# Kernel tuning notes

Measured on AMD Instinct MI355X. Metric: run time of the kernel, lower is better.

The kernel has to match this reference:

```python
import jax, jax.numpy as jnp
import numpy as np

IN_C = 128
KEY_C = 128
VAL_C = 128
HEADS = 8
N_CLS = 4

def setup_inputs() -> dict:
    key = jax.random.key(0)
    ks = jax.random.split(key, 10)
    n, c, d, h, w = 2, IN_C, 16, 64, 64
    x = jax.random.normal(ks[0], (n, c, d, h, w), dtype=jnp.float32)
    CLS = jax.random.normal(ks[1], (n, KEY_C, N_CLS), dtype=jnp.float32)
    s = 0.02
    Wk = jax.random.normal(ks[2], (KEY_C, IN_C), dtype=jnp.float32) * s
    bk = jnp.zeros((KEY_C,), dtype=jnp.float32)
    Wq = jax.random.normal(ks[3], (KEY_C, IN_C), dtype=jnp.float32) * s
    bq = jnp.zeros((KEY_C,), dtype=jnp.float32)
    Wv = jax.random.normal(ks[4], (VAL_C, IN_C), dtype=jnp.float32) * s
    bv = jnp.zeros((VAL_C,), dtype=jnp.float32)
    Wr = jax.random.normal(ks[5], (IN_C, VAL_C), dtype=jnp.float32) * s
    br = jnp.zeros((IN_C,), dtype=jnp.float32)
    return {"x": x, "CLS": CLS, "Wk": Wk, "bk": bk, "Wq": Wq, "bq": bq,
            "Wv": Wv, "bv": bv, "Wr": Wr, "br": br}

def reference(x, CLS, Wk, bk, Wq, bq, Wv, bv, Wr, br):
    n, c, d, h, w = x.shape
    L = d * h * w
    xf = x.reshape(n, c, L)
    # 1x1 Conv3d == channel matmul
    keys = jnp.einsum('oc,ncl->nol', Wk, xf) + bk[None, :, None]
    queries = jnp.einsum('oc,ncl->nol', Wq, xf) + bq[None, :, None]
    values = jnp.einsum('oc,ncl->nol', Wv, xf) + bv[None, :, None]
    # prepend CLS tokens along the sequence axis
    keys = jnp.concatenate([CLS, keys], axis=-1)      # (n, kc, L+4)
    queries = jnp.concatenate([CLS, queries], axis=-1)
    values = jnp.concatenate([CLS, values], axis=-1)
    Lt = L + N_CLS
    hk = KEY_C // HEADS
    hv = VAL_C // HEADS
    # contiguous channel slices per head == reshape (n, HEADS, hk, Lt)
    k = jax.nn.softmax(keys.reshape(n, HEADS, hk, Lt), axis=3)    # softmax over sequence
    q = jax.nn.softmax(queries.reshape(n, HEADS, hk, Lt), axis=2) # softmax over head channels
    v = values.reshape(n, HEADS, hv, Lt)
    context = jnp.einsum('nhkl,nhvl->nhkv', k, v)                 # (n, H, hk, hv)
    att = jnp.einsum('nhkv,nhkl->nhvl', context, q)               # (n, H, hv, Lt)
    # original loop reassigns CLS each head; final value comes from last head
    CLS_out = att[:, -1, :, :N_CLS]                               # (n, hv, 4)
    agg = att[:, :, :, N_CLS:].reshape(n, HEADS * hv, L)          # concat over heads
    attention = (jnp.einsum('oc,ncl->nol', Wr, agg) + br[None, :, None]).reshape(n, c, d, h, w)
    context_last = context[:, -1]                                 # last head's context
    return (attention, context_last, CLS_out)
```

## Files before the change

kernel.cpp:

```cpp
#include <hip/hip_runtime.h>

typedef unsigned short u16;
typedef short bf16x8 __attribute__((ext_vector_type(8)));
typedef float floatx4 __attribute__((ext_vector_type(4)));

#define L_TOT 65536
#define OUT_CTX 16777216
#define OUT_CLS (OUT_CTX + 512)

__device__ __forceinline__ u16 f2b(float f) {
  unsigned int u = __float_as_uint(f);
  u += 0x7fffu + ((u >> 16) & 1u);
  return (u16)(u >> 16);
}
__device__ __forceinline__ float blo(unsigned int u) { return __uint_as_float(u << 16); }
__device__ __forceinline__ float bhi(unsigned int u) { return __uint_as_float(u & 0xffff0000u); }

__device__ __forceinline__ float pack_val(const float* W, int eo) {
  int mt = eo >> 11;
  int rem = eo & 2047;
  int ks = rem >> 9;
  int lane = (rem >> 3) & 63;
  int j = rem & 7;
  int row = mt * 16 + (lane & 15);
  int col = ks * 32 + (lane >> 4) * 8 + j;
  return W[row * 128 + col];
}

__global__ __launch_bounds__(256) void kP(
    const float* __restrict__ Wk, const float* __restrict__ Wq,
    const float* __restrict__ Wv, const float* __restrict__ Wr,
    const float* __restrict__ CLS,
    float* __restrict__ S2, float* __restrict__ Cnum2,
    u16* __restrict__ wkv, u16* __restrict__ wqf, u16* __restrict__ wrf) {
  const int t = threadIdx.x;
  if (blockIdx.x < 32) {
    #pragma unroll
    for (int i = 0; i < 8; ++i) {
      int e = blockIdx.x * 2048 + i * 256 + t;
      if (e < 32768) {
        wkv[e] = f2b(pack_val(e < 16384 ? Wk : Wv, e & 16383));
      } else if (e < 49152) {
        int eq = e - 32768;
        wqf[eq] = f2b(pack_val(Wq, eq));
      } else {
        int er = e - 49152;
        wrf[er] = f2b(pack_val(Wr, er));
      }
    }
  } else {
    int n = t >> 7, r = t & 127;
    float s = 0.f;
    #pragma unroll
    for (int j = 0; j < 4; ++j) s += __expf(CLS[(n * 128 + r) * 4 + j]);
    S2[n * 128 + r] = s;
    S2[256 + n * 128 + r] = 0.f;
    for (int i = 0; i < 16; ++i) {
      int o = t * 16 + i;
      int nn = o >> 11;
      int rem = o & 2047;
      int h = rem >> 8;
      int kc = (rem >> 4) & 15;
      int vc = rem & 15;
      float a = 0.f;
      #pragma unroll
      for (int j = 0; j < 4; ++j)
        a += __expf(CLS[(nn * 128 + h * 16 + kc) * 4 + j]) *
             CLS[(nn * 128 + h * 16 + vc) * 4 + j];
      Cnum2[o] = a;
      Cnum2[4096 + o] = 0.f;
    }
  }
}

__global__ __launch_bounds__(256) void kA(
    const float* __restrict__ x, const float* __restrict__ bk,
    const float* __restrict__ bv, float* __restrict__ S2,
    float* __restrict__ Cnum2, const u16* __restrict__ wkv) {
  __shared__ __align__(16) u16 xT[64][136];
  __shared__ __align__(16) u16 ev[256][72];
  const int t = threadIdx.x;
  const int w = t >> 6, lane = t & 63;
  const int quad = lane >> 4, lm = lane & 15;
  const int n = blockIdx.x >> 8;
  const int l0base = (blockIdx.x & 255) << 8;
  const int slot = blockIdx.x & 1;

  const int sc = t >> 4;
  const int sl4 = t & 15;

  float4 pf[8];
  #pragma unroll
  for (int i = 0; i < 8; ++i) {
    int c = i * 16 + sc;
    pf[i] = *(const float4*)(x + (((size_t)(n * 128 + c)) << 16) + l0base + sl4 * 4);
  }

  bf16x8 wf[4][4];
  #pragma unroll
  for (int mt = 0; mt < 4; ++mt) {
    int rb = (mt < 2) ? (2 * w + mt) : (8 + 2 * w + (mt - 2));
    #pragma unroll
    for (int ks = 0; ks < 4; ++ks)
      wf[mt][ks] = *(const bf16x8*)(wkv + (((rb * 4 + ks) * 64 + lane) * 8));
  }
  float bias_[4][4];
  #pragma unroll
  for (int mt = 0; mt < 4; ++mt)
    #pragma unroll
    for (int j = 0; j < 4; ++j) {
      int r = w * 32 + (mt & 1) * 16 + quad * 4 + j;
      bias_[mt][j] = (mt < 2) ? bk[r] : bv[r];
    }

  floatx4 z4 = {0.f, 0.f, 0.f, 0.f};
  floatx4 cacc[2] = {z4, z4};
  float sacc = 0.f;

  for (int tile = 0; tile < 4; ++tile) {
    #pragma unroll
    for (int i = 0; i < 8; ++i) {
      int cc = i * 16 + sc;
      int col = sl4 * 4;
      xT[col + 0][cc] = f2b(pf[i].x);
      xT[col + 1][cc] = f2b(pf[i].y);
      xT[col + 2][cc] = f2b(pf[i].z);
      xT[col + 3][cc] = f2b(pf[i].w);
    }
    __syncthreads();

    floatx4 acc[4][4];
    #pragma unroll
    for (int mt = 0; mt < 4; ++mt)
      #pragma unroll
      for (int nt = 0; nt < 4; ++nt) acc[mt][nt] = z4;

    #pragma unroll
    for (int nt = 0; nt < 4; ++nt)
      #pragma unroll
      for (int ks = 0; ks < 4; ++ks) {
        bf16x8 b = *(const bf16x8*)(&xT[nt * 16 + lm][ks * 32 + quad * 8]);
        #pragma unroll
        for (int mt = 0; mt < 4; ++mt)
          acc[mt][nt] = __builtin_amdgcn_mfma_f32_16x16x32_bf16(wf[mt][ks], b, acc[mt][nt], 0, 0, 0);
      }

    #pragma unroll
    for (int mt = 0; mt < 4; ++mt)
      #pragma unroll
      for (int j = 0; j < 4; ++j) {
        int R = ((mt < 2) ? 0 : 128) + w * 32 + (mt & 1) * 16 + quad * 4 + j;
        #pragma unroll
        for (int nt = 0; nt < 4; ++nt) {
          float v = acc[mt][nt][j] + bias_[mt][j];
          if (mt < 2) v = __expf(v);
          ev[R][nt * 16 + lm] = f2b(v);
        }
      }

    if (tile < 3) {
      int l0 = l0base + (tile + 1) * 64;
      #pragma unroll
      for (int i = 0; i < 8; ++i) {
        int c = i * 16 + sc;
        pf[i] = *(const float4*)(x + (((size_t)(n * 128 + c)) << 16) + l0 + sl4 * 4);
      }
    }
    __syncthreads();

    #pragma unroll
    for (int hh = 0; hh < 2; ++hh) {
      int h = w * 2 + hh;
      #pragma unroll
      for (int ks = 0; ks < 2; ++ks) {
        bf16x8 aE = *(const bf16x8*)(&ev[h * 16 + lm][ks * 32 + quad * 8]);
        bf16x8 bV = *(const bf16x8*)(&ev[128 + h * 16 + lm][ks * 32 + quad * 8]);
        cacc[hh] = __builtin_amdgcn_mfma_f32_16x16x32_bf16(aE, bV, cacc[hh], 0, 0, 0);
      }
    }
    if (t < 128) {
      #pragma unroll
      for (int i = 0; i < 8; ++i) {
        uint4 u = *(const uint4*)(&ev[t][i * 8]);
        sacc += blo(u.x) + bhi(u.x) + blo(u.y) + bhi(u.y) +
                blo(u.z) + bhi(u.z) + blo(u.w) + bhi(u.w);
      }
    }
  }

  float* Cn = Cnum2 + slot * 4096;
  #pragma unroll
  for (int hh = 0; hh < 2; ++hh) {
    int h = w * 2 + hh;
    #pragma unroll
    for (int j = 0; j < 4; ++j)
      atomicAdd(&Cn[((n * 8 + h) * 16 + quad * 4 + j) * 16 + lm], cacc[hh][j]);
  }
  if (t < 128) atomicAdd(&S2[slot * 256 + n * 128 + t], sacc);
}

__global__ __launch_bounds__(256) void kB(
    const float* __restrict__ x, const float* __restrict__ bq,
    const float* __restrict__ br, const u16* __restrict__ wqf,
    const u16* __restrict__ wrf, const float* __restrict__ S2,
    const float* __restrict__ Cnum2, const float* __restrict__ CLS,
    float* __restrict__ out) {
  __shared__ __align__(16) u16 xT[64][136];
  __shared__ __align__(16) u16 qT[64][136];
  __shared__ __align__(16) u16 aT[64][136];
  const int t = threadIdx.x;
  const int w = t >> 6, lane = t & 63;
  const int quad = lane >> 4, lm = lane & 15;
  const int n = blockIdx.x >> 8;
  const int l0base = (blockIdx.x & 255) << 8;

  const int sc = t >> 4;
  const int sl4 = t & 15;

  float4 pf[8];
  #pragma unroll
  for (int i = 0; i < 8; ++i) {
    int c = i * 16 + sc;
    pf[i] = *(const float4*)(x + (((size_t)(n * 128 + c)) << 16) + l0base + sl4 * 4);
  }

  bf16x8 wq[2][4], wr[2][4];
  #pragma unroll
  for (int mt = 0; mt < 2; ++mt)
    #pragma unroll
    for (int ks = 0; ks < 4; ++ks) {
      wq[mt][ks] = *(const bf16x8*)(wqf + ((((w * 2 + mt) * 4 + ks) * 64 + lane) * 8));
      wr[mt][ks] = *(const bf16x8*)(wrf + ((((w * 2 + mt) * 4 + ks) * 64 + lane) * 8));
    }

  bf16x8 aC[2];
  #pragma unroll
  for (int mt = 0; mt < 2; ++mt) {
    int h = w * 2 + mt;
    short frag[8];
    #pragma unroll
    for (int j = 0; j < 8; ++j) {
      int k = quad * 8 + j;
      float v = 0.f;
      if (k < 16) {
        int ci = ((n * 8 + h) * 16 + k) * 16 + lm;
        float c = Cnum2[ci] + Cnum2[4096 + ci];
        float s = S2[n * 128 + h * 16 + k] + S2[256 + n * 128 + h * 16 + k];
        v = c / s;
      }
      frag[j] = (short)f2b(v);
    }
    aC[mt] = *(bf16x8*)frag;
  }

  if (blockIdx.x == 0) {
    for (int e = t; e < 512; e += 256) {
      int nn = e >> 8;
      int kc = (e >> 4) & 15;
      int vc = e & 15;
      int ci = ((nn * 8 + 7) * 16 + kc) * 16 + vc;
      float c = Cnum2[ci] + Cnum2[4096 + ci];
      float s = S2[nn * 128 + 112 + kc] + S2[256 + nn * 128 + 112 + kc];
      out[OUT_CTX + e] = c / s;
    }
    if (t < 128) {
      int nn = t >> 6;
      int vc = (t >> 2) & 15;
      int j = t & 3;
      float den = 0.f, num = 0.f;
      #pragma unroll
      for (int kc = 0; kc < 16; ++kc) {
        float e_ = __expf(CLS[(nn * 128 + 112 + kc) * 4 + j]);
        int ci = ((nn * 8 + 7) * 16 + kc) * 16 + vc;
        float c = Cnum2[ci] + Cnum2[4096 + ci];
        float s = S2[nn * 128 + 112 + kc] + S2[256 + nn * 128 + 112 + kc];
        den += e_;
        num += e_ * (c / s);
      }
      out[OUT_CLS + t] = num / den;
    }
  }

  float bqv_[2][4], brv[2][4];
  #pragma unroll
  for (int mt = 0; mt < 2; ++mt)
    #pragma unroll
    for (int j = 0; j < 4; ++j) {
      bqv_[mt][j] = bq[(w * 2 + mt) * 16 + quad * 4 + j];
      brv[mt][j] = br[(w * 2 + mt) * 16 + quad * 4 + j];
    }

  floatx4 z4 = {0.f, 0.f, 0.f, 0.f};

  for (int tile = 0; tile < 4; ++tile) {
    int l0 = l0base + tile * 64;
    #pragma unroll
    for (int i = 0; i < 8; ++i) {
      int cc = i * 16 + sc;
      int col = sl4 * 4;
      xT[col + 0][cc] = f2b(pf[i].x);
      xT[col + 1][cc] = f2b(pf[i].y);
      xT[col + 2][cc] = f2b(pf[i].z);
      xT[col + 3][cc] = f2b(pf[i].w);
    }
    __syncthreads();

    floatx4 acc[2][4];
    #pragma unroll
    for (int mt = 0; mt < 2; ++mt)
      #pragma unroll
      for (int nt = 0; nt < 4; ++nt) acc[mt][nt] = z4;

    #pragma unroll
    for (int nt = 0; nt < 4; ++nt)
      #pragma unroll
      for (int ks = 0; ks < 4; ++ks) {
        bf16x8 b = *(const bf16x8*)(&xT[nt * 16 + lm][ks * 32 + quad * 8]);
        #pragma unroll
        for (int mt = 0; mt < 2; ++mt)
          acc[mt][nt] = __builtin_amdgcn_mfma_f32_16x16x32_bf16(wq[mt][ks], b, acc[mt][nt], 0, 0, 0);
      }

    #pragma unroll
    for (int mt = 0; mt < 2; ++mt) {
      int h = w * 2 + mt;
      #pragma unroll
      for (int nt = 0; nt < 4; ++nt) {
        float e[4];
        float ssum = 0.f;
        #pragma unroll
        for (int j = 0; j < 4; ++j) {
          e[j] = __expf(acc[mt][nt][j] + bqv_[mt][j]);
          ssum += e[j];
        }
        ssum += __shfl_xor(ssum, 16);
        ssum += __shfl_xor(ssum, 32);
        float inv = 1.f / ssum;
        #pragma unroll
        for (int j = 0; j < 4; ++j)
          qT[nt * 16 + lm][h * 16 + quad * 4 + j] = f2b(e[j] * inv);
      }
    }

    #pragma unroll
    for (int mt = 0; mt < 2; ++mt) {
      int h = w * 2 + mt;
      #pragma unroll
      for (int nt = 0; nt < 4; ++nt) {
        bf16x8 bq_ = *(const bf16x8*)(&qT[nt * 16 + lm][h * 16 + (quad & 1) * 8]);
        floatx4 d = __builtin_amdgcn_mfma_f32_16x16x32_bf16(aC[mt], bq_, z4, 0, 0, 0);
        #pragma unroll
        for (int j = 0; j < 4; ++j)
          aT[nt * 16 + lm][h * 16 + quad * 4 + j] = f2b(d[j]);
      }
    }

    if (tile < 3) {
      int l0n = l0base + (tile + 1) * 64;
      #pragma unroll
      for (int i = 0; i < 8; ++i) {
        int c = i * 16 + sc;
        pf[i] = *(const float4*)(x + (((size_t)(n * 128 + c)) << 16) + l0n + sl4 * 4);
      }
    }
    __syncthreads();

    floatx4 acc2[2][4];
    #pragma unroll
    for (int mt = 0; mt < 2; ++mt)
      #pragma unroll
      for (int nt = 0; nt < 4; ++nt) acc2[mt][nt] = z4;

    #pragma unroll
    for (int nt = 0; nt < 4; ++nt)
      #pragma unroll
      for (int ks = 0; ks < 4; ++ks) {
        bf16x8 b = *(const bf16x8*)(&aT[nt * 16 + lm][ks * 32 + quad * 8]);
        #pragma unroll
        for (int mt = 0; mt < 2; ++mt)
          acc2[mt][nt] = __builtin_amdgcn_mfma_f32_16x16x32_bf16(wr[mt][ks], b, acc2[mt][nt], 0, 0, 0);
      }

    #pragma unroll
    for (int mt = 0; mt < 2; ++mt)
      #pragma unroll
      for (int j = 0; j < 4; ++j) {
        int R = (w * 2 + mt) * 16 + quad * 4 + j;
        #pragma unroll
        for (int nt = 0; nt < 4; ++nt)
          out[(((size_t)(n * 128 + R)) << 16) + l0 + nt * 16 + lm] = acc2[mt][nt][j] + brv[mt][j];
      }
  }
}

extern "C" void kernel_launch(void* const* d_in, const int* in_sizes, int n_in,
                              void* d_out, int out_size, void* d_ws, size_t ws_size,
                              hipStream_t stream) {
  const float* x   = (const float*)d_in[0];
  const float* CLS = (const float*)d_in[1];
  const float* Wk  = (const float*)d_in[2];
  const float* bk  = (const float*)d_in[3];
  const float* Wq  = (const float*)d_in[4];
  const float* bq  = (const float*)d_in[5];
  const float* Wv  = (const float*)d_in[6];
  const float* bv  = (const float*)d_in[7];
  const float* Wr  = (const float*)d_in[8];
  const float* br  = (const float*)d_in[9];
  float* out = (float*)d_out;
  char* ws = (char*)d_ws;
  float* S2    = (float*)(ws + 0);
  float* Cnum2 = (float*)(ws + 2048);
  u16* wkv     = (u16*)(ws + 34816);
  u16* wqf     = (u16*)(ws + 100352);
  u16* wrf     = (u16*)(ws + 133120);

  kP<<<33, 256, 0, stream>>>(Wk, Wq, Wv, Wr, CLS, S2, Cnum2, wkv, wqf, wrf);
  kA<<<512, 256, 0, stream>>>(x, bk, bv, S2, Cnum2, wkv);
  kB<<<512, 256, 0, stream>>>(x, bq, br, wqf, wrf, S2, Cnum2, CLS, out);
}
```

Before: 168.7 us.

## Fold context into output projection and double block count for attention kernels

Adds a small kernel kM that normalizes the accumulated context and folds it into the output projection weights (Wr·context per batch). This removes kB's per-tile context MFMA and the aT shared buffer, so the second GEMM consumes the softmaxed queries directly. Both main kernels now launch 1024 blocks of 128 positions each instead of 512 blocks of 256, with four atomic slots instead of two. kA computes the key-exp row sums from registers with shuffle reductions rather than rereading shared memory, and double-buffers xT so one barrier per tile can be dropped. The cost is an extra kernel launch and more atomics into four slots.

```diff
diff --git a/kernel.cpp b/kernel.cpp
--- a/kernel.cpp
+++ b/kernel.cpp
@@ -4,7 +4,6 @@
 typedef short bf16x8 __attribute__((ext_vector_type(8)));
 typedef float floatx4 __attribute__((ext_vector_type(4)));
 
-#define L_TOT 65536
 #define OUT_CTX 16777216
 #define OUT_CLS (OUT_CTX + 512)
 
@@ -13,8 +12,7 @@
   u += 0x7fffu + ((u >> 16) & 1u);
   return (u16)(u >> 16);
 }
-__device__ __forceinline__ float blo(unsigned int u) { return __uint_as_float(u << 16); }
-__device__ __forceinline__ float bhi(unsigned int u) { return __uint_as_float(u & 0xffff0000u); }
+__device__ __forceinline__ float b2f(u16 b) { return __uint_as_float(((unsigned int)b) << 16); }
 
 __device__ __forceinline__ float pack_val(const float* W, int eo) {
   int mt = eo >> 11;
@@ -29,35 +27,32 @@
 
 __global__ __launch_bounds__(256) void kP(
     const float* __restrict__ Wk, const float* __restrict__ Wq,
-    const float* __restrict__ Wv, const float* __restrict__ Wr,
-    const float* __restrict__ CLS,
+    const float* __restrict__ Wv, const float* __restrict__ CLS,
     float* __restrict__ S2, float* __restrict__ Cnum2,
-    u16* __restrict__ wkv, u16* __restrict__ wqf, u16* __restrict__ wrf) {
+    u16* __restrict__ wkv, u16* __restrict__ wqf) {
   const int t = threadIdx.x;
-  if (blockIdx.x < 32) {
+  if (blockIdx.x < 24) {
     #pragma unroll
     for (int i = 0; i < 8; ++i) {
       int e = blockIdx.x * 2048 + i * 256 + t;
       if (e < 32768) {
         wkv[e] = f2b(pack_val(e < 16384 ? Wk : Wv, e & 16383));
-      } else if (e < 49152) {
-        int eq = e - 32768;
-        wqf[eq] = f2b(pack_val(Wq, eq));
       } else {
-        int er = e - 49152;
-        wrf[er] = f2b(pack_val(Wr, er));
+        wqf[e - 32768] = f2b(pack_val(Wq, e - 32768));
       }
     }
   } else {
-    int n = t >> 7, r = t & 127;
+    int nn = t >> 7, r = t & 127;
     float s = 0.f;
     #pragma unroll
-    for (int j = 0; j < 4; ++j) s += __expf(CLS[(n * 128 + r) * 4 + j]);
-    S2[n * 128 + r] = s;
-    S2[256 + n * 128 + r] = 0.f;
+    for (int j = 0; j < 4; ++j) s += __expf(CLS[(nn * 128 + r) * 4 + j]);
+    S2[t] = s;
+    S2[256 + t] = 0.f;
+    S2[512 + t] = 0.f;
+    S2[768 + t] = 0.f;
     for (int i = 0; i < 16; ++i) {
       int o = t * 16 + i;
-      int nn = o >> 11;
+      int n2 = o >> 11;
       int rem = o & 2047;
       int h = rem >> 8;
       int kc = (rem >> 4) & 15;
@@ -65,10 +60,12 @@
       float a = 0.f;
       #pragma unroll
       for (int j = 0; j < 4; ++j)
-        a += __expf(CLS[(nn * 128 + h * 16 + kc) * 4 + j]) *
-             CLS[(nn * 128 + h * 16 + vc) * 4 + j];
+        a += __expf(CLS[(n2 * 128 + h * 16 + kc) * 4 + j]) *
+             CLS[(n2 * 128 + h * 16 + vc) * 4 + j];
       Cnum2[o] = a;
       Cnum2[4096 + o] = 0.f;
+      Cnum2[8192 + o] = 0.f;
+      Cnum2[12288 + o] = 0.f;
     }
   }
 }
@@ -77,15 +74,14 @@
     const float* __restrict__ x, const float* __restrict__ bk,
     const float* __restrict__ bv, float* __restrict__ S2,
     float* __restrict__ Cnum2, const u16* __restrict__ wkv) {
-  __shared__ __align__(16) u16 xT[64][136];
+  __shared__ __align__(16) u16 xT[2][64][136];
   __shared__ __align__(16) u16 ev[256][72];
   const int t = threadIdx.x;
   const int w = t >> 6, lane = t & 63;
   const int quad = lane >> 4, lm = lane & 15;
-  const int n = blockIdx.x >> 8;
-  const int l0base = (blockIdx.x & 255) << 8;
-  const int slot = blockIdx.x & 1;
-
+  const int n = blockIdx.x >> 9;
+  const int l0base = (blockIdx.x & 511) << 7;
+  const int slot = blockIdx.x & 3;
   const int sc = t >> 4;
   const int sl4 = t & 15;
 
@@ -115,9 +111,193 @@
 
   floatx4 z4 = {0.f, 0.f, 0.f, 0.f};
   floatx4 cacc[2] = {z4, z4};
-  float sacc = 0.f;
-
-  for (int tile = 0; tile < 4; ++tile) {
+  float sacc[2][4] = {{0.f, 0.f, 0.f, 0.f}, {0.f, 0.f, 0.f, 0.f}};
+
+  for (int tile = 0; tile < 2; ++tile) {
+    u16 (*xb)[136] = xT[tile];
+    #pragma unroll
+    for (int i = 0; i < 8; ++i) {
+      int cc = i * 16 + sc;
+      int col = sl4 * 4;
+      xb[col + 0][cc] = f2b(pf[i].x);
+      xb[col + 1][cc] = f2b(pf[i].y);
+      xb[col + 2][cc] = f2b(pf[i].z);
+      xb[col + 3][cc] = f2b(pf[i].w);
+    }
+    __syncthreads();
+
+    floatx4 acc[4][4];
+    #pragma unroll
+    for (int mt = 0; mt < 4; ++mt)
+      #pragma unroll
+      for (int nt = 0; nt < 4; ++nt) acc[mt][nt] = z4;
+
+    #pragma unroll
+    for (int nt = 0; nt < 4; ++nt)
+      #pragma unroll
+      for (int ks = 0; ks < 4; ++ks) {
+        bf16x8 b = *(const bf16x8*)(&xb[nt * 16 + lm][ks * 32 + quad * 8]);
+        #pragma unroll
+        for (int mt = 0; mt < 4; ++mt)
+          acc[mt][nt] = __builtin_amdgcn_mfma_f32_16x16x32_bf16(wf[mt][ks], b, acc[mt][nt], 0, 0, 0);
+      }
+
+    if (tile == 0) {
+      #pragma unroll
+      for (int i = 0; i < 8; ++i) {
+        int c = i * 16 + sc;
+        pf[i] = *(const float4*)(x + (((size_t)(n * 128 + c)) << 16) + l0base + 64 + sl4 * 4);
+      }
+    }
+
+    #pragma unroll
+    for (int mt = 0; mt < 4; ++mt)
+      #pragma unroll
+      for (int j = 0; j < 4; ++j) {
+        int R = ((mt < 2) ? 0 : 128) + w * 32 + (mt & 1) * 16 + quad * 4 + j;
+        #pragma unroll
+        for (int nt = 0; nt < 4; ++nt) {
+          float v = acc[mt][nt][j] + bias_[mt][j];
+          if (mt < 2) {
+            v = __expf(v);
+            u16 b = f2b(v);
+            ev[R][nt * 16 + lm] = b;
+            sacc[mt][j] += b2f(b);
+          } else {
+            ev[R][nt * 16 + lm] = f2b(v);
+          }
+        }
+      }
+
+    #pragma unroll
+    for (int hh = 0; hh < 2; ++hh) {
+      int h = w * 2 + hh;
+      #pragma unroll
+      for (int ks = 0; ks < 2; ++ks) {
+        bf16x8 aE = *(const bf16x8*)(&ev[h * 16 + lm][ks * 32 + quad * 8]);
+        bf16x8 bV = *(const bf16x8*)(&ev[128 + h * 16 + lm][ks * 32 + quad * 8]);
+        cacc[hh] = __builtin_amdgcn_mfma_f32_16x16x32_bf16(aE, bV, cacc[hh], 0, 0, 0);
+      }
+    }
+  }
+
+  float* Cn = Cnum2 + slot * 4096;
+  #pragma unroll
+  for (int hh = 0; hh < 2; ++hh) {
+    int h = w * 2 + hh;
+    #pragma unroll
+    for (int j = 0; j < 4; ++j)
+      atomicAdd(&Cn[((n * 8 + h) * 16 + quad * 4 + j) * 16 + lm], cacc[hh][j]);
+  }
+  #pragma unroll
+  for (int mt = 0; mt < 2; ++mt)
+    #pragma unroll
+    for (int j = 0; j < 4; ++j) {
+      float s = sacc[mt][j];
+      s += __shfl_xor(s, 1);
+      s += __shfl_xor(s, 2);
+      s += __shfl_xor(s, 4);
+      s += __shfl_xor(s, 8);
+      if (lm == 0)
+        atomicAdd(&S2[slot * 256 + n * 128 + w * 32 + mt * 16 + quad * 4 + j], s);
+    }
+}
+
+__global__ __launch_bounds__(256) void kM(
+    const float* __restrict__ Wr, const float* __restrict__ CLS,
+    const float* __restrict__ S2, const float* __restrict__ Cnum2,
+    u16* __restrict__ mfrag, float* __restrict__ out) {
+  __shared__ float ctxn[4096];
+  const int t = threadIdx.x;
+  float sinv = 1.f / (S2[t] + S2[256 + t] + S2[512 + t] + S2[768 + t]);
+  #pragma unroll
+  for (int i = 0; i < 16; ++i) {
+    int o = t * 16 + i;
+    ctxn[o] = (Cnum2[o] + Cnum2[4096 + o] + Cnum2[8192 + o] + Cnum2[12288 + o]) * sinv;
+  }
+  __syncthreads();
+
+  if (blockIdx.x == 0) {
+    for (int e = t; e < 512; e += 256) {
+      int nn = e >> 8, kc = (e >> 4) & 15, vc = e & 15;
+      out[OUT_CTX + e] = ctxn[((nn * 8 + 7) * 16 + kc) * 16 + vc];
+    }
+    if (t < 128) {
+      int nn = t >> 6, vc = (t >> 2) & 15, j = t & 3;
+      float den = 0.f, num = 0.f;
+      #pragma unroll
+      for (int kc = 0; kc < 16; ++kc) {
+        float e_ = __expf(CLS[(nn * 128 + 112 + kc) * 4 + j]);
+        den += e_;
+        num += e_ * ctxn[((nn * 8 + 7) * 16 + kc) * 16 + vc];
+      }
+      out[OUT_CLS + t] = num / den;
+    }
+  }
+
+  #pragma unroll
+  for (int i = 0; i < 8; ++i) {
+    int e = blockIdx.x * 2048 + i * 256 + t;
+    int nn = e >> 14;
+    int rem = e & 16383;
+    int rb = rem >> 11;
+    int ks = (rem >> 9) & 3;
+    int ln = (rem >> 3) & 63;
+    int j = rem & 7;
+    int o = rb * 16 + (ln & 15);
+    int cc = ks * 32 + (ln >> 4) * 8 + j;
+    int h = cc >> 4, k = cc & 15;
+    float m = 0.f;
+    #pragma unroll
+    for (int v = 0; v < 16; ++v)
+      m += Wr[o * 128 + h * 16 + v] * ctxn[((nn * 8 + h) * 16 + k) * 16 + v];
+    mfrag[e] = f2b(m);
+  }
+}
+
+__global__ __launch_bounds__(256) void kB(
+    const float* __restrict__ x, const float* __restrict__ bq,
+    const float* __restrict__ br, const u16* __restrict__ wqf,
+    const u16* __restrict__ mfrag, float* __restrict__ out) {
+  __shared__ __align__(16) u16 xT[64][136];
+  __shared__ __align__(16) u16 qT[64][136];
+  const int t = threadIdx.x;
+  const int w = t >> 6, lane = t & 63;
+  const int quad = lane >> 4, lm = lane & 15;
+  const int n = blockIdx.x >> 9;
+  const int l0base = (blockIdx.x & 511) << 7;
+  const int sc = t >> 4;
+  const int sl4 = t & 15;
+
+  float4 pf[8];
+  #pragma unroll
+  for (int i = 0; i < 8; ++i) {
+    int c = i * 16 + sc;
+    pf[i] = *(const float4*)(x + (((size_t)(n * 128 + c)) << 16) + l0base + sl4 * 4);
+  }
+
+  bf16x8 wq[2][4], mA[2][4];
+  #pragma unroll
+  for (int mt = 0; mt < 2; ++mt)
+    #pragma unroll
+    for (int ks = 0; ks < 4; ++ks) {
+      wq[mt][ks] = *(const bf16x8*)(wqf + ((((w * 2 + mt) * 4 + ks) * 64 + lane) * 8));
+      mA[mt][ks] = *(const bf16x8*)(mfrag + ((((n * 8 + w * 2 + mt) * 4 + ks) * 64 + lane) * 8));
+    }
+
+  float bqv_[2][4], brv[2][4];
+  #pragma unroll
+  for (int mt = 0; mt < 2; ++mt)
+    #pragma unroll
+    for (int j = 0; j < 4; ++j) {
+      bqv_[mt][j] = bq[(w * 2 + mt) * 16 + quad * 4 + j];
+      brv[mt][j] = br[(w * 2 + mt) * 16 + quad * 4 + j];
+    }
+
+  floatx4 z4 = {0.f, 0.f, 0.f, 0.f};
+
+  for (int tile = 0; tile < 2; ++tile) {
+    int l0 = l0base + tile * 64;
     #pragma unroll
     for (int i = 0; i < 8; ++i) {
       int cc = i * 16 + sc;
@@ -129,182 +309,6 @@
     }
     __syncthreads();
 
-    floatx4 acc[4][4];
-    #pragma unroll
-    for (int mt = 0; mt < 4; ++mt)
-      #pragma unroll
-      for (int nt = 0; nt < 4; ++nt) acc[mt][nt] = z4;
-
-    #pragma unroll
-    for (int nt = 0; nt < 4; ++nt)
-      #pragma unroll
-      for (int ks = 0; ks < 4; ++ks) {
-        bf16x8 b = *(const bf16x8*)(&xT[nt * 16 + lm][ks * 32 + quad * 8]);
-        #pragma unroll
-        for (int mt = 0; mt < 4; ++mt)
-          acc[mt][nt] = __builtin_amdgcn_mfma_f32_16x16x32_bf16(wf[mt][ks], b, acc[mt][nt], 0, 0, 0);
-      }
-
-    #pragma unroll
-    for (int mt = 0; mt < 4; ++mt)
-      #pragma unroll
-      for (int j = 0; j < 4; ++j) {
-        int R = ((mt < 2) ? 0 : 128) + w * 32 + (mt & 1) * 16 + quad * 4 + j;
-        #pragma unroll
-        for (int nt = 0; nt < 4; ++nt) {
-          float v = acc[mt][nt][j] + bias_[mt][j];
-          if (mt < 2) v = __expf(v);
-          ev[R][nt * 16 + lm] = f2b(v);
-        }
-      }
-
-    if (tile < 3) {
-      int l0 = l0base + (tile + 1) * 64;
-      #pragma unroll
-      for (int i = 0; i < 8; ++i) {
-        int c = i * 16 + sc;
-        pf[i] = *(const float4*)(x + (((size_t)(n * 128 + c)) << 16) + l0 + sl4 * 4);
-      }
-    }
-    __syncthreads();
-
-    #pragma unroll
-    for (int hh = 0; hh < 2; ++hh) {
-      int h = w * 2 + hh;
-      #pragma unroll
-      for (int ks = 0; ks < 2; ++ks) {
-        bf16x8 aE = *(const bf16x8*)(&ev[h * 16 + lm][ks * 32 + quad * 8]);
-        bf16x8 bV = *(const bf16x8*)(&ev[128 + h * 16 + lm][ks * 32 + quad * 8]);
-        cacc[hh] = __builtin_amdgcn_mfma_f32_16x16x32_bf16(aE, bV, cacc[hh], 0, 0, 0);
-      }
-    }
-    if (t < 128) {
-      #pragma unroll
-      for (int i = 0; i < 8; ++i) {
-        uint4 u = *(const uint4*)(&ev[t][i * 8]);
-        sacc += blo(u.x) + bhi(u.x) + blo(u.y) + bhi(u.y) +
-                blo(u.z) + bhi(u.z) + blo(u.w) + bhi(u.w);
-      }
-    }
-  }
-
-  float* Cn = Cnum2 + slot * 4096;
-  #pragma unroll
-  for (int hh = 0; hh < 2; ++hh) {
-    int h = w * 2 + hh;
-    #pragma unroll
-    for (int j = 0; j < 4; ++j)
-      atomicAdd(&Cn[((n * 8 + h) * 16 + quad * 4 + j) * 16 + lm], cacc[hh][j]);
-  }
-  if (t < 128) atomicAdd(&S2[slot * 256 + n * 128 + t], sacc);
-}
-
-__global__ __launch_bounds__(256) void kB(
-    const float* __restrict__ x, const float* __restrict__ bq,
-    const float* __restrict__ br, const u16* __restrict__ wqf,
-    const u16* __restrict__ wrf, const float* __restrict__ S2,
-    const float* __restrict__ Cnum2, const float* __restrict__ CLS,
-    float* __restrict__ out) {
-  __shared__ __align__(16) u16 xT[64][136];
-  __shared__ __align__(16) u16 qT[64][136];
-  __shared__ __align__(16) u16 aT[64][136];
-  const int t = threadIdx.x;
-  const int w = t >> 6, lane = t & 63;
-  const int quad = lane >> 4, lm = lane & 15;
-  const int n = blockIdx.x >> 8;
-  const int l0base = (blockIdx.x & 255) << 8;
-
-  const int sc = t >> 4;
-  const int sl4 = t & 15;
-
-  float4 pf[8];
-  #pragma unroll
-  for (int i = 0; i < 8; ++i) {
-    int c = i * 16 + sc;
-    pf[i] = *(const float4*)(x + (((size_t)(n * 128 + c)) << 16) + l0base + sl4 * 4);
-  }
-
-  bf16x8 wq[2][4], wr[2][4];
-  #pragma unroll
-  for (int mt = 0; mt < 2; ++mt)
-    #pragma unroll
-    for (int ks = 0; ks < 4; ++ks) {
-      wq[mt][ks] = *(const bf16x8*)(wqf + ((((w * 2 + mt) * 4 + ks) * 64 + lane) * 8));
-      wr[mt][ks] = *(const bf16x8*)(wrf + ((((w * 2 + mt) * 4 + ks) * 64 + lane) * 8));
-    }
-
-  bf16x8 aC[2];
-  #pragma unroll
-  for (int mt = 0; mt < 2; ++mt) {
-    int h = w * 2 + mt;
-    short frag[8];
-    #pragma unroll
-    for (int j = 0; j < 8; ++j) {
-      int k = quad * 8 + j;
-      float v = 0.f;
-      if (k < 16) {
-        int ci = ((n * 8 + h) * 16 + k) * 16 + lm;
-        float c = Cnum2[ci] + Cnum2[4096 + ci];
-        float s = S2[n * 128 + h * 16 + k] + S2[256 + n * 128 + h * 16 + k];
-        v = c / s;
-      }
-      frag[j] = (short)f2b(v);
-    }
-    aC[mt] = *(bf16x8*)frag;
-  }
-
-  if (blockIdx.x == 0) {
-    for (int e = t; e < 512; e += 256) {
-      int nn = e >> 8;
-      int kc = (e >> 4) & 15;
-      int vc = e & 15;
-      int ci = ((nn * 8 + 7) * 16 + kc) * 16 + vc;
-      float c = Cnum2[ci] + Cnum2[4096 + ci];
-      float s = S2[nn * 128 + 112 + kc] + S2[256 + nn * 128 + 112 + kc];
-      out[OUT_CTX + e] = c / s;
-    }
-    if (t < 128) {
-      int nn = t >> 6;
-      int vc = (t >> 2) & 15;
-      int j = t & 3;
-      float den = 0.f, num = 0.f;
-      #pragma unroll
-      for (int kc = 0; kc < 16; ++kc) {
-        float e_ = __expf(CLS[(nn * 128 + 112 + kc) * 4 + j]);
-        int ci = ((nn * 8 + 7) * 16 + kc) * 16 + vc;
-        float c = Cnum2[ci] + Cnum2[4096 + ci];
-        float s = S2[nn * 128 + 112 + kc] + S2[256 + nn * 128 + 112 + kc];
-        den += e_;
-        num += e_ * (c / s);
-      }
-      out[OUT_CLS + t] = num / den;
-    }
-  }
-
-  float bqv_[2][4], brv[2][4];
-  #pragma unroll
-  for (int mt = 0; mt < 2; ++mt)
-    #pragma unroll
-    for (int j = 0; j < 4; ++j) {
-      bqv_[mt][j] = bq[(w * 2 + mt) * 16 + quad * 4 + j];
-      brv[mt][j] = br[(w * 2 + mt) * 16 + quad * 4 + j];
-    }
-
-  floatx4 z4 = {0.f, 0.f, 0.f, 0.f};
-
-  for (int tile = 0; tile < 4; ++tile) {
-    int l0 = l0base + tile * 64;
-    #pragma unroll
-    for (int i = 0; i < 8; ++i) {
-      int cc = i * 16 + sc;
-      int col = sl4 * 4;
-      xT[col + 0][cc] = f2b(pf[i].x);
-      xT[col + 1][cc] = f2b(pf[i].y);
-      xT[col + 2][cc] = f2b(pf[i].z);
-      xT[col + 3][cc] = f2b(pf[i].w);
-    }
-    __syncthreads();
-
     floatx4 acc[2][4];
     #pragma unroll
     for (int mt = 0; mt < 2; ++mt)
@@ -342,25 +346,11 @@
       }
     }
 
-    #pragma unroll
-    for (int mt = 0; mt < 2; ++mt) {
-      int h = w * 2 + mt;
-      #pragma unroll
-      for (int nt = 0; nt < 4; ++nt) {
-        bf16x8 bq_ = *(const bf16x8*)(&qT[nt * 16 + lm][h * 16 + (quad & 1) * 8]);
-        floatx4 d = __builtin_amdgcn_mfma_f32_16x16x32_bf16(aC[mt], bq_, z4, 0, 0, 0);
-        #pragma unroll
-        for (int j = 0; j < 4; ++j)
-          aT[nt * 16 + lm][h * 16 + quad * 4 + j] = f2b(d[j]);
-      }
-    }
-
-    if (tile < 3) {
-      int l0n = l0base + (tile + 1) * 64;
+    if (tile == 0) {
       #pragma unroll
       for (int i = 0; i < 8; ++i) {
         int c = i * 16 + sc;
-        pf[i] = *(const float4*)(x + (((size_t)(n * 128 + c)) << 16) + l0n + sl4 * 4);
+        pf[i] = *(const float4*)(x + (((size_t)(n * 128 + c)) << 16) + l0base + 64 + sl4 * 4);
       }
     }
     __syncthreads();
@@ -375,10 +365,10 @@
     for (int nt = 0; nt < 4; ++nt)
       #pragma unroll
       for (int ks = 0; ks < 4; ++ks) {
-        bf16x8 b = *(const bf16x8*)(&aT[nt * 16 + lm][ks * 32 + quad * 8]);
+        bf16x8 b = *(const bf16x8*)(&qT[nt * 16 + lm][ks * 32 + quad * 8]);
         #pragma unroll
         for (int mt = 0; mt < 2; ++mt)
-          acc2[mt][nt] = __builtin_amdgcn_mfma_f32_16x16x32_bf16(wr[mt][ks], b, acc2[mt][nt], 0, 0, 0);
+          acc2[mt][nt] = __builtin_amdgcn_mfma_f32_16x16x32_bf16(mA[mt][ks], b, acc2[mt][nt], 0, 0, 0);
       }
 
     #pragma unroll
@@ -409,12 +399,13 @@
   float* out = (float*)d_out;
   char* ws = (char*)d_ws;
   float* S2    = (float*)(ws + 0);
-  float* Cnum2 = (float*)(ws + 2048);
-  u16* wkv     = (u16*)(ws + 34816);
-  u16* wqf     = (u16*)(ws + 100352);
-  u16* wrf     = (u16*)(ws + 133120);
-
-  kP<<<33, 256, 0, stream>>>(Wk, Wq, Wv, Wr, CLS, S2, Cnum2, wkv, wqf, wrf);
-  kA<<<512, 256, 0, stream>>>(x, bk, bv, S2, Cnum2, wkv);
-  kB<<<512, 256, 0, stream>>>(x, bq, br, wqf, wrf, S2, Cnum2, CLS, out);
-}
+  float* Cnum2 = (float*)(ws + 4096);
+  u16* wkv     = (u16*)(ws + 69632);
+  u16* wqf     = (u16*)(ws + 135168);
+  u16* mfrag   = (u16*)(ws + 167936);
+
+  kP<<<25, 256, 0, stream>>>(Wk, Wq, Wv, CLS, S2, Cnum2, wkv, wqf);
+  kA<<<1024, 256, 0, stream>>>(x, bk, bv, S2, Cnum2, wkv);
+  kM<<<16, 256, 0, stream>>>(Wr, CLS, S2, Cnum2, mfrag, out);
+  kB<<<1024, 256, 0, stream>>>(x, bq, br, wqf, mfrag, out);
+}
```

After: 195.8 us. 16.0% more time.
